# Optimization experiments

Hardware: AMD Instinct MI355X
Metric: run time of the kernel (lower is better)

## Reference

```python
import jax, jax.numpy as jnp
import numpy as np

N_NODES = 50000
N_EDGES = 1600000
N_EDGE_F = 128
GLOBAL_F = 64
N_GRAPHS = 512
HIDDEN = N_EDGE_F // 2


def setup_inputs() -> dict:
    key = jax.random.key(0)
    k = jax.random.split(key, 8)
    x = jax.random.normal(k[0], (N_NODES, N_EDGE_F), dtype=jnp.float32)
    edge_index = jax.random.randint(k[1], (2, N_EDGES), 0, N_NODES, dtype=jnp.int64)
    edge_attr = jax.random.normal(k[2], (N_EDGES, N_EDGE_F), dtype=jnp.float32)
    u = jax.random.normal(k[3], (N_GRAPHS, GLOBAL_F), dtype=jnp.float32)
    batch = jnp.sort(jax.random.randint(k[4], (N_NODES,), 0, N_GRAPHS, dtype=jnp.int64))
    # MLP params (Linear1: in=n_edge_f+global_f, out=hidden; Linear2: hidden -> global_f)
    in1 = N_EDGE_F + GLOBAL_F
    W1 = jax.random.normal(k[5], (in1, HIDDEN), dtype=jnp.float32) / np.sqrt(in1)
    b1 = jnp.zeros((HIDDEN,), dtype=jnp.float32)
    W2 = jax.random.normal(k[6], (HIDDEN, GLOBAL_F), dtype=jnp.float32) / np.sqrt(HIDDEN)
    b2 = jnp.zeros((GLOBAL_F,), dtype=jnp.float32)
    return {"x": x, "edge_index": edge_index, "edge_attr": edge_attr, "u": u,
            "batch": batch, "W1": W1, "b1": b1, "W2": W2, "b2": b2}


def reference(x, edge_index, edge_attr, u, batch, W1, b1, W2, b2):
    # graph id of each edge = graph id of its source node
    seg = batch[edge_index[0]]                                   # [E]
    sums = jax.ops.segment_sum(edge_attr, seg, num_segments=N_GRAPHS)  # [B, n_edge_f]
    counts = jax.ops.segment_sum(jnp.ones((edge_attr.shape[0],), edge_attr.dtype),
                                 seg, num_segments=N_GRAPHS)
    mean = sums / jnp.maximum(counts, 1.0)[:, None]              # scatter-mean (0 for empty)
    out = jnp.concatenate([u, mean], axis=1)                     # [B, global_f + n_edge_f]
    # dropout in eval mode == identity
    h = jax.nn.relu(out @ W1 + b1)
    return h @ W2 + b2
```

## Files before the change

kernel.cpp:

```cpp
#include <hip/hip_runtime.h>
#include <hip/hip_bf16.h>

using u32 = unsigned int;
using u16 = unsigned short;

#define NGR   512
#define NF    128
#define GF    64
#define HID   64
#define IN1   192

#define HT    256
#define ITEMS 10
#define EPB   (HT * ITEMS)

__global__ void zero_counts_kernel(u32* __restrict__ counts) {
    counts[threadIdx.x] = 0u;
}

__global__ void hist_kernel(const int* __restrict__ ei0,
                            const int* __restrict__ batch,
                            u32* __restrict__ g_counts, int E) {
    __shared__ u32 h[NGR];
    int tid = threadIdx.x;
    h[tid] = 0u; h[tid + 256] = 0u;
    __syncthreads();
    int base = blockIdx.x * EPB + tid;
#pragma unroll
    for (int i = 0; i < ITEMS; ++i) {
        int e = base + i * HT;
        if (e < E) {
            int s = batch[ei0[e]];
            atomicAdd(&h[s], 1u);
        }
    }
    __syncthreads();
    u32 v0 = h[tid];       if (v0) atomicAdd(&g_counts[tid], v0);
    u32 v1 = h[tid + 256]; if (v1) atomicAdd(&g_counts[tid + 256], v1);
}

__global__ void scan_kernel(const u32* __restrict__ counts,
                            u32* __restrict__ offsets,
                            u32* __restrict__ cursor) {
    __shared__ u32 A[NGR], B[NGR];
    int t = threadIdx.x;
    u32 c = counts[t];
    A[t] = c;
    __syncthreads();
    u32* src = A; u32* dst = B;
    for (int off = 1; off < NGR; off <<= 1) {
        u32 v = src[t];
        if (t >= off) v += src[t - off];
        dst[t] = v;
        __syncthreads();
        u32* tmp = src; src = dst; dst = tmp;
    }
    u32 exc = src[t] - c;
    offsets[t] = exc;
    cursor[t]  = exc;
}

__global__ void scatter_kernel(const int* __restrict__ ei0,
                               const int* __restrict__ batch,
                               u32* __restrict__ cursor,
                               u32* __restrict__ sorted, int E) {
    __shared__ u32 h[NGR];
    __shared__ u32 bs[NGR];
    int tid = threadIdx.x;
    h[tid] = 0u; h[tid + 256] = 0u;
    __syncthreads();
    int base = blockIdx.x * EPB + tid;
    u16 segs[ITEMS];
    u16 ranks[ITEMS];
#pragma unroll
    for (int i = 0; i < ITEMS; ++i) {
        int e = base + i * HT;
        if (e < E) {
            int s = batch[ei0[e]];
            segs[i]  = (u16)s;
            ranks[i] = (u16)atomicAdd(&h[s], 1u);
        }
    }
    __syncthreads();
    u32 v0 = h[tid];       if (v0) bs[tid]       = atomicAdd(&cursor[tid], v0);
    u32 v1 = h[tid + 256]; if (v1) bs[tid + 256] = atomicAdd(&cursor[tid + 256], v1);
    __syncthreads();
#pragma unroll
    for (int i = 0; i < ITEMS; ++i) {
        int e = base + i * HT;
        if (e < E) {
            sorted[bs[segs[i]] + ranks[i]] = (u32)e;
        }
    }
}

__launch_bounds__(512, 1)
__global__ void reduce_mlp_kernel(const float* __restrict__ edge_attr,
                                  const u32* __restrict__ sorted,
                                  const u32* __restrict__ counts,
                                  const u32* __restrict__ offsets,
                                  const float* __restrict__ u,
                                  const float* __restrict__ W1,
                                  const float* __restrict__ b1,
                                  const float* __restrict__ W2,
                                  const float* __restrict__ b2,
                                  float* __restrict__ out) {
    __shared__ float sW1[IN1 * HID];
    __shared__ float sW2[HID * GF];
    __shared__ float sb1[HID];
    __shared__ float sb2[GF];
    __shared__ float red[16 * NF];
    __shared__ float vin[IN1];
    __shared__ float hv[HID];

    int tid = threadIdx.x;
    int b   = blockIdx.x;

    for (int i = tid; i < IN1 * HID; i += 512) sW1[i] = W1[i];
    for (int i = tid; i < HID * GF;  i += 512) sW2[i] = W2[i];
    if (tid < HID) sb1[tid] = b1[tid];
    if (tid < GF)  { sb2[tid] = b2[tid]; vin[tid] = u[b * GF + tid]; }

    u32 off = offsets[b];
    u32 cnt = counts[b];
    int row  = tid >> 5;
    int lane = tid & 31;

    float4 a0 = make_float4(0.f, 0.f, 0.f, 0.f);
    float4 a1 = a0, a2 = a0, a3 = a0;

    u32 j = (u32)row;
    for (; j + 48 < cnt; j += 64) {
        u32 e0 = sorted[off + j];
        u32 e1 = sorted[off + j + 16];
        u32 e2 = sorted[off + j + 32];
        u32 e3 = sorted[off + j + 48];
        float4 v0 = ((const float4*)(edge_attr + (size_t)e0 * NF))[lane];
        float4 v1 = ((const float4*)(edge_attr + (size_t)e1 * NF))[lane];
        float4 v2 = ((const float4*)(edge_attr + (size_t)e2 * NF))[lane];
        float4 v3 = ((const float4*)(edge_attr + (size_t)e3 * NF))[lane];
        a0.x += v0.x; a0.y += v0.y; a0.z += v0.z; a0.w += v0.w;
        a1.x += v1.x; a1.y += v1.y; a1.z += v1.z; a1.w += v1.w;
        a2.x += v2.x; a2.y += v2.y; a2.z += v2.z; a2.w += v2.w;
        a3.x += v3.x; a3.y += v3.y; a3.z += v3.z; a3.w += v3.w;
    }
    for (; j < cnt; j += 16) {
        u32 e = sorted[off + j];
        float4 v = ((const float4*)(edge_attr + (size_t)e * NF))[lane];
        a0.x += v.x; a0.y += v.y; a0.z += v.z; a0.w += v.w;
    }
    a0.x += a1.x + a2.x + a3.x;
    a0.y += a1.y + a2.y + a3.y;
    a0.z += a1.z + a2.z + a3.z;
    a0.w += a1.w + a2.w + a3.w;
    ((float4*)red)[row * 32 + lane] = a0;
    __syncthreads();

    if (tid < NF) {
        float s = 0.f;
#pragma unroll
        for (int r = 0; r < 16; ++r) s += red[r * NF + tid];
        vin[GF + tid] = s / fmaxf((float)cnt, 1.0f);
    }
    __syncthreads();

    if (tid < HID) {
        float acc = sb1[tid];
#pragma unroll
        for (int k = 0; k < IN1; ++k) acc += vin[k] * sW1[k * HID + tid];
        hv[tid] = fmaxf(acc, 0.0f);
    }
    __syncthreads();

    if (tid < GF) {
        float acc = sb2[tid];
#pragma unroll
        for (int k = 0; k < HID; ++k) acc += hv[k] * sW2[k * GF + tid];
        out[b * GF + tid] = acc;
    }
}

extern "C" void kernel_launch(void* const* d_in, const int* in_sizes, int n_in,
                              void* d_out, int out_size, void* d_ws, size_t ws_size,
                              hipStream_t stream) {
    const int*   ei        = (const int*)d_in[1];
    const float* edge_attr = (const float*)d_in[2];
    const float* u         = (const float*)d_in[3];
    const int*   batch     = (const int*)d_in[4];
    const float* W1        = (const float*)d_in[5];
    const float* b1        = (const float*)d_in[6];
    const float* W2        = (const float*)d_in[7];
    const float* b2        = (const float*)d_in[8];
    float*       out       = (float*)d_out;

    const int E = in_sizes[1] / 2;
    const int* ei0 = ei;

    u32* sorted  = (u32*)d_ws;
    u32* counts  = sorted + E;
    u32* offsets = counts + NGR;
    u32* cursor  = offsets + NGR;

    const int nblocks = (E + EPB - 1) / EPB;

    zero_counts_kernel<<<1, NGR, 0, stream>>>(counts);
    hist_kernel<<<nblocks, HT, 0, stream>>>(ei0, batch, counts, E);
    scan_kernel<<<1, NGR, 0, stream>>>(counts, offsets, cursor);
    scatter_kernel<<<nblocks, HT, 0, stream>>>(ei0, batch, cursor, sorted, E);
    reduce_mlp_kernel<<<NGR, 512, 0, stream>>>(edge_attr, sorted, counts, offsets,
                                               u, W1, b1, W2, b2, out);
}
```

Before: 212.5 us.

## Split per-graph reduction across blocks and cache segment ids from histogram

After: 214.0 us. About the same (+0.7%).

```diff
diff --git a/kernel.cpp b/kernel.cpp
--- a/kernel.cpp
+++ b/kernel.cpp
@@ -9,6 +9,7 @@
 #define GF    64
 #define HID   64
 #define IN1   192
+#define SPLIT 8
 
 #define HT    256
 #define ITEMS 10
@@ -20,7 +21,8 @@
 
 __global__ void hist_kernel(const int* __restrict__ ei0,
                             const int* __restrict__ batch,
-                            u32* __restrict__ g_counts, int E) {
+                            u32* __restrict__ g_counts,
+                            u16* __restrict__ seg, int E) {
     __shared__ u32 h[NGR];
     int tid = threadIdx.x;
     h[tid] = 0u; h[tid + 256] = 0u;
@@ -31,6 +33,7 @@
         int e = base + i * HT;
         if (e < E) {
             int s = batch[ei0[e]];
+            seg[e] = (u16)s;
             atomicAdd(&h[s], 1u);
         }
     }
@@ -60,8 +63,7 @@
     cursor[t]  = exc;
 }
 
-__global__ void scatter_kernel(const int* __restrict__ ei0,
-                               const int* __restrict__ batch,
+__global__ void scatter_kernel(const u16* __restrict__ seg,
                                u32* __restrict__ cursor,
                                u32* __restrict__ sorted, int E) {
     __shared__ u32 h[NGR];
@@ -76,7 +78,7 @@
     for (int i = 0; i < ITEMS; ++i) {
         int e = base + i * HT;
         if (e < E) {
-            int s = batch[ei0[e]];
+            int s = seg[e];
             segs[i]  = (u16)s;
             ranks[i] = (u16)atomicAdd(&h[s], 1u);
         }
@@ -94,47 +96,34 @@
     }
 }
 
-__launch_bounds__(512, 1)
-__global__ void reduce_mlp_kernel(const float* __restrict__ edge_attr,
-                                  const u32* __restrict__ sorted,
-                                  const u32* __restrict__ counts,
-                                  const u32* __restrict__ offsets,
-                                  const float* __restrict__ u,
-                                  const float* __restrict__ W1,
-                                  const float* __restrict__ b1,
-                                  const float* __restrict__ W2,
-                                  const float* __restrict__ b2,
-                                  float* __restrict__ out) {
-    __shared__ float sW1[IN1 * HID];
-    __shared__ float sW2[HID * GF];
-    __shared__ float sb1[HID];
-    __shared__ float sb2[GF];
-    __shared__ float red[16 * NF];
-    __shared__ float vin[IN1];
-    __shared__ float hv[HID];
-
+__launch_bounds__(256, 8)
+__global__ void reduce_kernel(const float* __restrict__ edge_attr,
+                              const u32* __restrict__ sorted,
+                              const u32* __restrict__ counts,
+                              const u32* __restrict__ offsets,
+                              float* __restrict__ partial) {
+    __shared__ float red[8 * NF];
     int tid = threadIdx.x;
-    int b   = blockIdx.x;
-
-    for (int i = tid; i < IN1 * HID; i += 512) sW1[i] = W1[i];
-    for (int i = tid; i < HID * GF;  i += 512) sW2[i] = W2[i];
-    if (tid < HID) sb1[tid] = b1[tid];
-    if (tid < GF)  { sb2[tid] = b2[tid]; vin[tid] = u[b * GF + tid]; }
-
-    u32 off = offsets[b];
-    u32 cnt = counts[b];
+    int g   = blockIdx.x >> 3;
+    int s   = blockIdx.x & (SPLIT - 1);
+    u32 off = offsets[g];
+    u32 cnt = counts[g];
+    u32 chunk = (cnt + SPLIT - 1) / SPLIT;
+    u32 start = (u32)s * chunk;
+    u32 end   = min(cnt, start + chunk);
+
     int row  = tid >> 5;
     int lane = tid & 31;
 
     float4 a0 = make_float4(0.f, 0.f, 0.f, 0.f);
     float4 a1 = a0, a2 = a0, a3 = a0;
 
-    u32 j = (u32)row;
-    for (; j + 48 < cnt; j += 64) {
+    u32 j = start + (u32)row;
+    for (; j + 24 < end; j += 32) {
         u32 e0 = sorted[off + j];
-        u32 e1 = sorted[off + j + 16];
-        u32 e2 = sorted[off + j + 32];
-        u32 e3 = sorted[off + j + 48];
+        u32 e1 = sorted[off + j + 8];
+        u32 e2 = sorted[off + j + 16];
+        u32 e3 = sorted[off + j + 24];
         float4 v0 = ((const float4*)(edge_attr + (size_t)e0 * NF))[lane];
         float4 v1 = ((const float4*)(edge_attr + (size_t)e1 * NF))[lane];
         float4 v2 = ((const float4*)(edge_attr + (size_t)e2 * NF))[lane];
@@ -144,7 +133,7 @@
         a2.x += v2.x; a2.y += v2.y; a2.z += v2.z; a2.w += v2.w;
         a3.x += v3.x; a3.y += v3.y; a3.z += v3.z; a3.w += v3.w;
     }
-    for (; j < cnt; j += 16) {
+    for (; j < end; j += 8) {
         u32 e = sorted[off + j];
         float4 v = ((const float4*)(edge_attr + (size_t)e * NF))[lane];
         a0.x += v.x; a0.y += v.y; a0.z += v.z; a0.w += v.w;
@@ -157,26 +146,45 @@
     __syncthreads();
 
     if (tid < NF) {
+        float v = 0.f;
+#pragma unroll
+        for (int r = 0; r < 8; ++r) v += red[r * NF + tid];
+        partial[(size_t)blockIdx.x * NF + tid] = v;
+    }
+}
+
+__global__ void final_kernel(const float* __restrict__ partial,
+                             const u32* __restrict__ counts,
+                             const float* __restrict__ u,
+                             const float* __restrict__ W1,
+                             const float* __restrict__ b1,
+                             const float* __restrict__ W2,
+                             const float* __restrict__ b2,
+                             float* __restrict__ out) {
+    __shared__ float vin[IN1];
+    __shared__ float hv[HID];
+    int b = blockIdx.x, t = threadIdx.x;
+    if (t < NF) {
         float s = 0.f;
 #pragma unroll
-        for (int r = 0; r < 16; ++r) s += red[r * NF + tid];
-        vin[GF + tid] = s / fmaxf((float)cnt, 1.0f);
-    }
-    __syncthreads();
-
-    if (tid < HID) {
-        float acc = sb1[tid];
-#pragma unroll
-        for (int k = 0; k < IN1; ++k) acc += vin[k] * sW1[k * HID + tid];
-        hv[tid] = fmaxf(acc, 0.0f);
-    }
-    __syncthreads();
-
-    if (tid < GF) {
-        float acc = sb2[tid];
-#pragma unroll
-        for (int k = 0; k < HID; ++k) acc += hv[k] * sW2[k * GF + tid];
-        out[b * GF + tid] = acc;
+        for (int r = 0; r < SPLIT; ++r)
+            s += partial[(size_t)(b * SPLIT + r) * NF + t];
+        vin[GF + t] = s / fmaxf((float)counts[b], 1.0f);
+    }
+    if (t < GF) vin[t] = u[b * GF + t];
+    __syncthreads();
+    if (t < HID) {
+        float acc = b1[t];
+#pragma unroll
+        for (int k = 0; k < IN1; ++k) acc += vin[k] * W1[k * HID + t];
+        hv[t] = fmaxf(acc, 0.0f);
+    }
+    __syncthreads();
+    if (t < GF) {
+        float acc = b2[t];
+#pragma unroll
+        for (int k = 0; k < HID; ++k) acc += hv[k] * W2[k * GF + t];
+        out[b * GF + t] = acc;
     }
 }
 
@@ -196,17 +204,20 @@
     const int E = in_sizes[1] / 2;
     const int* ei0 = ei;
 
-    u32* sorted  = (u32*)d_ws;
-    u32* counts  = sorted + E;
-    u32* offsets = counts + NGR;
-    u32* cursor  = offsets + NGR;
+    u32*   sorted  = (u32*)d_ws;
+    float* partial = (float*)(sorted + E);
+    u32*   counts  = (u32*)(partial + (size_t)NGR * SPLIT * NF);
+    u32*   offsets = counts + NGR;
+    u32*   cursor  = offsets + NGR;
+    u16*   seg     = (u16*)(cursor + NGR);
 
     const int nblocks = (E + EPB - 1) / EPB;
 
     zero_counts_kernel<<<1, NGR, 0, stream>>>(counts);
-    hist_kernel<<<nblocks, HT, 0, stream>>>(ei0, batch, counts, E);
+    hist_kernel<<<nblocks, HT, 0, stream>>>(ei0, batch, counts, seg, E);
     scan_kernel<<<1, NGR, 0, stream>>>(counts, offsets, cursor);
-    scatter_kernel<<<nblocks, HT, 0, stream>>>(ei0, batch, cursor, sorted, E);
-    reduce_mlp_kernel<<<NGR, 512, 0, stream>>>(edge_attr, sorted, counts, offsets,
-                                               u, W1, b1, W2, b2, out);
-}
+    scatter_kernel<<<nblocks, HT, 0, stream>>>(seg, cursor, sorted, E);
+    reduce_kernel<<<NGR * SPLIT, 256, 0, stream>>>(edge_attr, sorted, counts,
+                                                   offsets, partial);
+    final_kernel<<<NGR, 128, 0, stream>>>(partial, counts, u, W1, b1, W2, b2, out);
+}
```
